# Optimization experiments

Hardware: AMD Instinct MI355X
Metric: run time of the kernel (lower is better)

## Reference

```python
import jax, jax.numpy as jnp
import numpy as np

H = 32  # hidden_size
T = 7   # num_day (seq_len)
F = 1   # num_feature
B = 262144


def _glorot(key, shape):
    # mimic torch uniform(-1/sqrt(H), 1/sqrt(H)) init for LSTM/Linear params
    bound = 1.0 / np.sqrt(H)
    return jax.random.uniform(key, shape, jnp.float32, -bound, bound)


def setup_inputs() -> dict:
    key = jax.random.key(0)
    ks = jax.random.split(key, 14)
    return {
        "inputs": jax.random.normal(ks[0], (B, T, F), jnp.float32),
        # layer 0 (input_size=F)
        "W_ih0": _glorot(ks[1], (4 * H, F)),
        "W_hh0": _glorot(ks[2], (4 * H, H)),
        "b_ih0": _glorot(ks[3], (4 * H,)),
        "b_hh0": _glorot(ks[4], (4 * H,)),
        # layer 1 (input_size=H)
        "W_ih1": _glorot(ks[5], (4 * H, H)),
        "W_hh1": _glorot(ks[6], (4 * H, H)),
        "b_ih1": _glorot(ks[7], (4 * H,)),
        "b_hh1": _glorot(ks[8], (4 * H,)),
        # fc: Linear(H, 1)
        "fc_w": _glorot(ks[9], (1, H)),
        "fc_b": _glorot(ks[10], (1,)),
        # fc1: Linear(T, 1)
        "fc1_w": jax.random.uniform(ks[11], (1, T), jnp.float32, -1.0 / np.sqrt(T), 1.0 / np.sqrt(T)),
        "fc1_b": jax.random.uniform(ks[12], (1,), jnp.float32, -1.0 / np.sqrt(T), 1.0 / np.sqrt(T)),
    }


def _lstm_layer(x_tbf, W_ih, W_hh, b):
    # x_tbf: [T, B, in]; PyTorch gate order: i, f, g, o
    Bdim = x_tbf.shape[1]
    h0 = jnp.zeros((Bdim, H), x_tbf.dtype)
    c0 = jnp.zeros((Bdim, H), x_tbf.dtype)

    def step(carry, x_t):
        h, c = carry
        gates = x_t @ W_ih.T + h @ W_hh.T + b  # [B, 4H]
        i, f, g, o = jnp.split(gates, 4, axis=-1)
        i = jax.nn.sigmoid(i)
        f = jax.nn.sigmoid(f)
        g = jnp.tanh(g)
        o = jax.nn.sigmoid(o)
        c = f * c + i * g
        h = o * jnp.tanh(c)
        return (h, c), h

    _, hs = jax.lax.scan(step, (h0, c0), x_tbf)
    return hs  # [T, B, H]


def reference(inputs, W_ih0, W_hh0, b_ih0, b_hh0, W_ih1, W_hh1, b_ih1, b_hh1,
              fc_w, fc_b, fc1_w, fc1_b):
    x = jnp.transpose(inputs, (1, 0, 2))            # [T, B, F]
    h1 = _lstm_layer(x, W_ih0, W_hh0, b_ih0 + b_hh0)  # [T, B, H]
    h2 = _lstm_layer(h1, W_ih1, W_hh1, b_ih1 + b_hh1)  # [T, B, H]
    out = jnp.transpose(h2, (1, 0, 2))              # [B, T, H]
    y = out @ fc_w.T + fc_b                          # [B, T, 1]
    y = jnp.squeeze(y, 2)                            # [B, T]
    y = y @ fc1_w.T + fc1_b                          # [B, 1]
    return y
```

## Files before the change

### kernel.cpp

```cpp
#include <hip/hip_runtime.h>


#define HID 32
#define TSTEPS 7
#define LSTRIDE 36
#define NWAVES 8

typedef _Float16 half8 __attribute__((ext_vector_type(8)));
typedef float floatx4 __attribute__((ext_vector_type(4)));
typedef float floatx2 __attribute__((ext_vector_type(2)));

#define LOG2E 1.44269504088896f

__device__ __forceinline__ float fast_rcp(float x) { return __builtin_amdgcn_rcpf(x); }

__device__ __forceinline__ float exp2_fast(float x) {
#if __has_builtin(__builtin_amdgcn_exp2f)
    return __builtin_amdgcn_exp2f(x);
#else
    return __expf(x * 0.69314718055994531f);
#endif
}

__device__ __forceinline__ floatx2 mk2(float a, float b) {
    floatx2 v; v[0] = a; v[1] = b; return v;
}
__device__ __forceinline__ floatx2 exp2_v2(floatx2 a) {
    return mk2(exp2_fast(a[0]), exp2_fast(a[1]));
}

__device__ __forceinline__ floatx2 cell_pair(floatx2 gi, floatx2 gf,
                                             floatx2 gg, floatx2 go,
                                             floatx2& cst) {
    const floatx2 one = mk2(1.0f, 1.0f);
    const floatx2 Ea = exp2_v2(gi);
    const floatx2 Db = exp2_v2(gf) + one;
    const floatx2 Ed = exp2_v2(gg);
    const floatx2 Ee = exp2_v2(go);
    const floatx2 M  = (Ea + one) * (Ed + one);
    const float Rb = fast_rcp(Db[0] * Db[1]);
    const float Rm = fast_rcp(M[0] * M[1]);
    const floatx2 ff  = mk2(Rb, Rb) * mk2(Db[1], Db[0]);
    const floatx2 rig = mk2(Rm, Rm) * mk2(M[1], M[0]);
    const floatx2 ig  = __builtin_elementwise_fma(Ed, rig, -rig);
    const floatx2 c   = __builtin_elementwise_fma(ff, cst, ig);
    cst = c;
    const floatx2 Ec  = exp2_v2(c * mk2(2.0f * LOG2E, 2.0f * LOG2E));
    const floatx2 Dh  = (Ee + one) * (Ec + one);
    const float Rh = fast_rcp(Dh[0] * Dh[1]);
    const floatx2 th = mk2(Rh, Rh) * mk2(Dh[1], Dh[0]);
    return __builtin_elementwise_fma(Ec, th, -th);
}

__global__ __launch_bounds__(512, 2) void lstm2_mfma(
    const float* __restrict__ xin,
    const float* __restrict__ Wih0,
    const float* __restrict__ Whh0,
    const float* __restrict__ bih0,
    const float* __restrict__ bhh0,
    const float* __restrict__ Wih1,
    const float* __restrict__ Whh1,
    const float* __restrict__ bih1,
    const float* __restrict__ bhh1,
    const float* __restrict__ fcw,
    const float* __restrict__ fcb,
    const float* __restrict__ fc1w,
    const float* __restrict__ fc1b,
    float* __restrict__ out,
    int B)
{
    const int lane = threadIdx.x & 63;
    const int wave = threadIdx.x >> 6;
    const int col  = lane & 15;
    const int rg   = lane >> 4;
    const int seq_base = (blockIdx.x * NWAVES + wave) * 16;

    __shared__ __align__(16) _Float16 ldsw[3 * 8 * 64 * 8];
    __shared__ __align__(16) floatx2  ldsbw0[128];
    __shared__ float                  ldsb1[128];
    __shared__ __align__(16) _Float16 ldsh[NWAVES][16 * LSTRIDE];
    __shared__ __align__(16) float    ldsx[NWAVES][TSTEPS * 16];

    _Float16* hl = &ldsh[wave][0];
    float* xl = &ldsx[wave][0];

#pragma unroll
    for (int e = lane; e < TSTEPS * 16; e += 64) {
        const int s = e / TSTEPS;
        const int tt = e - s * TSTEPS;
        xl[tt * 16 + s] = xin[seq_base * TSTEPS + e];
    }

    if (wave < 3) {
        const float* Wsrc = (wave == 0) ? Whh0 : (wave == 1) ? Wih1 : Whh1;
#pragma unroll
        for (int nt = 0; nt < 8; ++nt) {
            const int n = nt * 16 + col;
            const float sc = ((n >> 5) == 2) ? (2.0f * LOG2E) : (-LOG2E);
            const float* s = Wsrc + n * HID + rg * 8;
            half8 f;
#pragma unroll
            for (int j = 0; j < 8; ++j) f[j] = (_Float16)(sc * s[j]);
            *(half8*)&ldsw[((wave * 8 + nt) * 64 + lane) * 8] = f;
        }
    } else if (wave == 3) {
#pragma unroll
        for (int i = 0; i < 2; ++i) {
            const int n = i * 64 + lane;
            const float sc = ((n >> 5) == 2) ? (2.0f * LOG2E) : (-LOG2E);
            floatx2 bw;
            bw[0] = sc * (bih0[n] + bhh0[n]);
            bw[1] = sc * Wih0[n];
            ldsbw0[n] = bw;
            ldsb1[n]  = sc * (bih1[n] + bhh1[n]);
        }
    }
    __syncthreads();

    const float fcw_l0 = fcw[col];
    const float fcw_l1 = fcw[16 + col];

    half8 Ah2 = {};
    floatx2 c1v[2][2] = {}, c2v[2][2] = {};
    floatx2 faccv[2] = {};

    floatx4 g0c[8];
    {
        const floatx4 xr0 = *(const floatx4*)&xl[rg * 4];
        const char* bB0p = (const char*)ldsbw0 + col * 8;
#pragma unroll
        for (int nt = 0; nt < 8; ++nt) {
            const floatx2 bw = *(const floatx2*)(bB0p + nt * 128);
#pragma unroll
            for (int r = 0; r < 4; ++r) g0c[nt][r] = fmaf(bw[1], xr0[r], bw[0]);
        }
    }

    for (int t = 0; t < TSTEPS; ++t) {
        unsigned woff = 0;
        asm volatile("" : "+v"(woff));
        const char* wB  = (const char*)ldsw   + lane * 16 + woff;
        const char* bB0 = (const char*)ldsbw0 + col * 8  + woff;
        const char* bB1 = (const char*)ldsb1  + col * 4  + woff;

#pragma unroll
        for (int q = 0; q < 2; ++q) {
#pragma unroll
            for (int rp = 0; rp < 2; ++rp) {
                const floatx2 h = cell_pair(
                    mk2(g0c[0 + q][rp * 2], g0c[0 + q][rp * 2 + 1]),
                    mk2(g0c[2 + q][rp * 2], g0c[2 + q][rp * 2 + 1]),
                    mk2(g0c[4 + q][rp * 2], g0c[4 + q][rp * 2 + 1]),
                    mk2(g0c[6 + q][rp * 2], g0c[6 + q][rp * 2 + 1]),
                    c1v[q][rp]);
                hl[(rg * 4 + rp * 2 + 0) * LSTRIDE + q * 16 + col] = (_Float16)h[0];
                hl[(rg * 4 + rp * 2 + 1) * LSTRIDE + q * 16 + col] = (_Float16)h[1];
            }
        }
        const half8 Ah1 = *(const half8*)&hl[col * LSTRIDE + rg * 8];

        floatx4 g1[8];
#pragma unroll
        for (int nt = 0; nt < 8; ++nt) {
            const float b1  = *(const float*)(bB1 + nt * 64);
            const half8 f1a = *(const half8*)(wB + 8192  + nt * 1024);
            const half8 f1b = *(const half8*)(wB + 16384 + nt * 1024);
            floatx4 c = {b1, b1, b1, b1};
            c = __builtin_amdgcn_mfma_f32_16x16x32_f16(Ah1, f1a, c, 0, 0, 0);
            g1[nt] = __builtin_amdgcn_mfma_f32_16x16x32_f16(Ah2, f1b, c, 0, 0, 0);
        }

        if (t + 1 < TSTEPS) {
            const floatx4 xr = *(const floatx4*)&xl[(t + 1) * 16 + rg * 4];
#pragma unroll
            for (int nt = 0; nt < 8; ++nt) {
                const floatx2 bw = *(const floatx2*)(bB0 + nt * 128);
                const half8 bf   = *(const half8*)(wB + nt * 1024);
                floatx4 c;
#pragma unroll
                for (int r = 0; r < 4; ++r) c[r] = fmaf(bw[1], xr[r], bw[0]);
                g0c[nt] = __builtin_amdgcn_mfma_f32_16x16x32_f16(Ah1, bf, c, 0, 0, 0);
            }
        }

        const float f1t = fc1w[t];
        const float w0 = f1t * fcw_l0;
        const float w1 = f1t * fcw_l1;
#pragma unroll
        for (int q = 0; q < 2; ++q) {
            const float wq = q ? w1 : w0;
            const floatx2 wqv = mk2(wq, wq);
#pragma unroll
            for (int rp = 0; rp < 2; ++rp) {
                const floatx2 h = cell_pair(
                    mk2(g1[0 + q][rp * 2], g1[0 + q][rp * 2 + 1]),
                    mk2(g1[2 + q][rp * 2], g1[2 + q][rp * 2 + 1]),
                    mk2(g1[4 + q][rp * 2], g1[4 + q][rp * 2 + 1]),
                    mk2(g1[6 + q][rp * 2], g1[6 + q][rp * 2 + 1]),
                    c2v[q][rp]);
                faccv[rp] = __builtin_elementwise_fma(wqv, h, faccv[rp]);
                hl[(rg * 4 + rp * 2 + 0) * LSTRIDE + q * 16 + col] = (_Float16)h[0];
                hl[(rg * 4 + rp * 2 + 1) * LSTRIDE + q * 16 + col] = (_Float16)h[1];
            }
        }
        Ah2 = *(const half8*)&hl[col * LSTRIDE + rg * 8];
    }

    float facc[4];
#pragma unroll
    for (int r = 0; r < 4; ++r) facc[r] = faccv[r >> 1][r & 1];
#pragma unroll
    for (int r = 0; r < 4; ++r) {
        float v = facc[r];
        v += __shfl_xor(v, 1);
        v += __shfl_xor(v, 2);
        v += __shfl_xor(v, 4);
        v += __shfl_xor(v, 8);
        facc[r] = v;
    }
    float sum_f1 = 0.f;
#pragma unroll
    for (int t = 0; t < TSTEPS; ++t) sum_f1 += fc1w[t];
    const float tail = fcb[0] * sum_f1 + fc1b[0];

    if (col == 0) {
#pragma unroll
        for (int r = 0; r < 4; ++r)
            out[seq_base + rg * 4 + r] = facc[r] + tail;
    }
}

extern "C" void kernel_launch(void* const* d_in, const int* in_sizes, int n_in,
                              void* d_out, int out_size, void* d_ws, size_t ws_size,
                              hipStream_t stream) {
    const float* xin  = (const float*)d_in[0];
    const float* Wih0 = (const float*)d_in[1];
    const float* Whh0 = (const float*)d_in[2];
    const float* bih0 = (const float*)d_in[3];
    const float* bhh0 = (const float*)d_in[4];
    const float* Wih1 = (const float*)d_in[5];
    const float* Whh1 = (const float*)d_in[6];
    const float* bih1 = (const float*)d_in[7];
    const float* bhh1 = (const float*)d_in[8];
    const float* fcw  = (const float*)d_in[9];
    const float* fcb  = (const float*)d_in[10];
    const float* fc1w = (const float*)d_in[11];
    const float* fc1b = (const float*)d_in[12];
    float* out = (float*)d_out;

    const int B = in_sizes[0] / TSTEPS;
    const int grid = B / (NWAVES * 16);
    lstm2_mfma<<<grid, NWAVES * 64, 0, stream>>>(
        xin, Wih0, Whh0, bih0, bhh0, Wih1, Whh1, bih1, bhh1,
        fcw, fcb, fc1w, fc1b, out, B);
}
```

Baseline: 197.1 us.

## Split LSTM layers across producer/consumer waves with double-buffered hidden state

Each block now processes 64 sequences with 8 waves split into two roles: waves 0-3 compute layer 0 and write h1 into a double-buffered LDS slot, while waves 4-7 consume it to compute layer 1 and the fc reduction. A block-wide barrier each timestep hands h1 from producer to consumer. This pipelines the two layers across waves and lowers per-wave register pressure. In exchange it halves sequences per block, doubles the grid, and adds seven __syncthreads per block.

Result: slower. 203.9 us (+3.4%).

```diff
diff --git a/kernel.cpp b/kernel.cpp
--- a/kernel.cpp
+++ b/kernel.cpp
@@ -4,7 +4,6 @@
 #define HID 32
 #define TSTEPS 7
 #define LSTRIDE 36
-#define NWAVES 8
 
 typedef _Float16 half8 __attribute__((ext_vector_type(8)));
 typedef float floatx4 __attribute__((ext_vector_type(4)));
@@ -71,24 +70,29 @@
 {
     const int lane = threadIdx.x & 63;
     const int wave = threadIdx.x >> 6;
+    const int pair = wave & 3;
+    const int role = wave >> 2;
     const int col  = lane & 15;
     const int rg   = lane >> 4;
-    const int seq_base = (blockIdx.x * NWAVES + wave) * 16;
+    const int seq_base = (blockIdx.x * 4 + pair) * 16;
 
     __shared__ __align__(16) _Float16 ldsw[3 * 8 * 64 * 8];
     __shared__ __align__(16) floatx2  ldsbw0[128];
     __shared__ float                  ldsb1[128];
-    __shared__ __align__(16) _Float16 ldsh[NWAVES][16 * LSTRIDE];
-    __shared__ __align__(16) float    ldsx[NWAVES][TSTEPS * 16];
-
-    _Float16* hl = &ldsh[wave][0];
-    float* xl = &ldsx[wave][0];
-
-#pragma unroll
-    for (int e = lane; e < TSTEPS * 16; e += 64) {
-        const int s = e / TSTEPS;
-        const int tt = e - s * TSTEPS;
-        xl[tt * 16 + s] = xin[seq_base * TSTEPS + e];
+    __shared__ __align__(16) _Float16 ldsh1[4][2][16 * LSTRIDE];
+    __shared__ __align__(16) _Float16 ldsh2[4][16 * LSTRIDE];
+    __shared__ __align__(16) float    ldsx[4][TSTEPS * 16];
+
+    float* xl = &ldsx[pair][0];
+    _Float16* h2l = &ldsh2[pair][0];
+
+    if (role == 0) {
+#pragma unroll
+        for (int e = lane; e < TSTEPS * 16; e += 64) {
+            const int s = e / TSTEPS;
+            const int tt = e - s * TSTEPS;
+            xl[tt * 16 + s] = xin[seq_base * TSTEPS + e];
+        }
     }
 
     if (wave < 3) {
@@ -120,21 +124,9 @@
     const float fcw_l0 = fcw[col];
     const float fcw_l1 = fcw[16 + col];
 
-    half8 Ah2 = {};
-    floatx2 c1v[2][2] = {}, c2v[2][2] = {};
-    floatx2 faccv[2] = {};
-
-    floatx4 g0c[8];
-    {
-        const floatx4 xr0 = *(const floatx4*)&xl[rg * 4];
-        const char* bB0p = (const char*)ldsbw0 + col * 8;
-#pragma unroll
-        for (int nt = 0; nt < 8; ++nt) {
-            const floatx2 bw = *(const floatx2*)(bB0p + nt * 128);
-#pragma unroll
-            for (int r = 0; r < 4; ++r) g0c[nt][r] = fmaf(bw[1], xr0[r], bw[0]);
-        }
-    }
+    half8 Acur = {};
+    floatx2 cv[2][2] = {};
+    floatx2 fv[2] = {};
 
     for (int t = 0; t < TSTEPS; ++t) {
         unsigned woff = 0;
@@ -143,35 +135,10 @@
         const char* bB0 = (const char*)ldsbw0 + col * 8  + woff;
         const char* bB1 = (const char*)ldsb1  + col * 4  + woff;
 
-#pragma unroll
-        for (int q = 0; q < 2; ++q) {
-#pragma unroll
-            for (int rp = 0; rp < 2; ++rp) {
-                const floatx2 h = cell_pair(
-                    mk2(g0c[0 + q][rp * 2], g0c[0 + q][rp * 2 + 1]),
-                    mk2(g0c[2 + q][rp * 2], g0c[2 + q][rp * 2 + 1]),
-                    mk2(g0c[4 + q][rp * 2], g0c[4 + q][rp * 2 + 1]),
-                    mk2(g0c[6 + q][rp * 2], g0c[6 + q][rp * 2 + 1]),
-                    c1v[q][rp]);
-                hl[(rg * 4 + rp * 2 + 0) * LSTRIDE + q * 16 + col] = (_Float16)h[0];
-                hl[(rg * 4 + rp * 2 + 1) * LSTRIDE + q * 16 + col] = (_Float16)h[1];
-            }
-        }
-        const half8 Ah1 = *(const half8*)&hl[col * LSTRIDE + rg * 8];
-
-        floatx4 g1[8];
-#pragma unroll
-        for (int nt = 0; nt < 8; ++nt) {
-            const float b1  = *(const float*)(bB1 + nt * 64);
-            const half8 f1a = *(const half8*)(wB + 8192  + nt * 1024);
-            const half8 f1b = *(const half8*)(wB + 16384 + nt * 1024);
-            floatx4 c = {b1, b1, b1, b1};
-            c = __builtin_amdgcn_mfma_f32_16x16x32_f16(Ah1, f1a, c, 0, 0, 0);
-            g1[nt] = __builtin_amdgcn_mfma_f32_16x16x32_f16(Ah2, f1b, c, 0, 0, 0);
-        }
-
-        if (t + 1 < TSTEPS) {
-            const floatx4 xr = *(const floatx4*)&xl[(t + 1) * 16 + rg * 4];
+        if (role == 0) {
+            _Float16* h1b = &ldsh1[pair][t & 1][0];
+            const floatx4 xr = *(const floatx4*)&xl[t * 16 + rg * 4];
+            floatx4 g[8];
 #pragma unroll
             for (int nt = 0; nt < 8; ++nt) {
                 const floatx2 bw = *(const floatx2*)(bB0 + nt * 128);
@@ -179,54 +146,87 @@
                 floatx4 c;
 #pragma unroll
                 for (int r = 0; r < 4; ++r) c[r] = fmaf(bw[1], xr[r], bw[0]);
-                g0c[nt] = __builtin_amdgcn_mfma_f32_16x16x32_f16(Ah1, bf, c, 0, 0, 0);
-            }
-        }
-
-        const float f1t = fc1w[t];
-        const float w0 = f1t * fcw_l0;
-        const float w1 = f1t * fcw_l1;
-#pragma unroll
-        for (int q = 0; q < 2; ++q) {
-            const float wq = q ? w1 : w0;
-            const floatx2 wqv = mk2(wq, wq);
-#pragma unroll
-            for (int rp = 0; rp < 2; ++rp) {
-                const floatx2 h = cell_pair(
-                    mk2(g1[0 + q][rp * 2], g1[0 + q][rp * 2 + 1]),
-                    mk2(g1[2 + q][rp * 2], g1[2 + q][rp * 2 + 1]),
-                    mk2(g1[4 + q][rp * 2], g1[4 + q][rp * 2 + 1]),
-                    mk2(g1[6 + q][rp * 2], g1[6 + q][rp * 2 + 1]),
-                    c2v[q][rp]);
-                faccv[rp] = __builtin_elementwise_fma(wqv, h, faccv[rp]);
-                hl[(rg * 4 + rp * 2 + 0) * LSTRIDE + q * 16 + col] = (_Float16)h[0];
-                hl[(rg * 4 + rp * 2 + 1) * LSTRIDE + q * 16 + col] = (_Float16)h[1];
-            }
-        }
-        Ah2 = *(const half8*)&hl[col * LSTRIDE + rg * 8];
-    }
-
-    float facc[4];
-#pragma unroll
-    for (int r = 0; r < 4; ++r) facc[r] = faccv[r >> 1][r & 1];
-#pragma unroll
-    for (int r = 0; r < 4; ++r) {
-        float v = facc[r];
-        v += __shfl_xor(v, 1);
-        v += __shfl_xor(v, 2);
-        v += __shfl_xor(v, 4);
-        v += __shfl_xor(v, 8);
-        facc[r] = v;
-    }
-    float sum_f1 = 0.f;
-#pragma unroll
-    for (int t = 0; t < TSTEPS; ++t) sum_f1 += fc1w[t];
-    const float tail = fcb[0] * sum_f1 + fc1b[0];
-
-    if (col == 0) {
-#pragma unroll
-        for (int r = 0; r < 4; ++r)
-            out[seq_base + rg * 4 + r] = facc[r] + tail;
+                g[nt] = __builtin_amdgcn_mfma_f32_16x16x32_f16(Acur, bf, c, 0, 0, 0);
+            }
+#pragma unroll
+            for (int q = 0; q < 2; ++q) {
+#pragma unroll
+                for (int rp = 0; rp < 2; ++rp) {
+                    const floatx2 h = cell_pair(
+                        mk2(g[0 + q][rp * 2], g[0 + q][rp * 2 + 1]),
+                        mk2(g[2 + q][rp * 2], g[2 + q][rp * 2 + 1]),
+                        mk2(g[4 + q][rp * 2], g[4 + q][rp * 2 + 1]),
+                        mk2(g[6 + q][rp * 2], g[6 + q][rp * 2 + 1]),
+                        cv[q][rp]);
+                    h1b[(rg * 4 + rp * 2 + 0) * LSTRIDE + q * 16 + col] = (_Float16)h[0];
+                    h1b[(rg * 4 + rp * 2 + 1) * LSTRIDE + q * 16 + col] = (_Float16)h[1];
+                }
+            }
+            Acur = *(const half8*)&h1b[col * LSTRIDE + rg * 8];
+        }
+
+        __syncthreads();
+
+        if (role == 1) {
+            const _Float16* h1b = &ldsh1[pair][t & 1][0];
+            const half8 Ah1t = *(const half8*)&h1b[col * LSTRIDE + rg * 8];
+            floatx4 g[8];
+#pragma unroll
+            for (int nt = 0; nt < 8; ++nt) {
+                const float b1  = *(const float*)(bB1 + nt * 64);
+                const half8 f1a = *(const half8*)(wB + 8192  + nt * 1024);
+                const half8 f1b = *(const half8*)(wB + 16384 + nt * 1024);
+                floatx4 c = {b1, b1, b1, b1};
+                c = __builtin_amdgcn_mfma_f32_16x16x32_f16(Ah1t, f1a, c, 0, 0, 0);
+                g[nt] = __builtin_amdgcn_mfma_f32_16x16x32_f16(Acur, f1b, c, 0, 0, 0);
+            }
+            const float f1t = fc1w[t];
+            const float w0 = f1t * fcw_l0;
+            const float w1 = f1t * fcw_l1;
+#pragma unroll
+            for (int q = 0; q < 2; ++q) {
+                const float wq = q ? w1 : w0;
+                const floatx2 wqv = mk2(wq, wq);
+#pragma unroll
+                for (int rp = 0; rp < 2; ++rp) {
+                    const floatx2 h = cell_pair(
+                        mk2(g[0 + q][rp * 2], g[0 + q][rp * 2 + 1]),
+                        mk2(g[2 + q][rp * 2], g[2 + q][rp * 2 + 1]),
+                        mk2(g[4 + q][rp * 2], g[4 + q][rp * 2 + 1]),
+                        mk2(g[6 + q][rp * 2], g[6 + q][rp * 2 + 1]),
+                        cv[q][rp]);
+                    fv[rp] = __builtin_elementwise_fma(wqv, h, fv[rp]);
+                    h2l[(rg * 4 + rp * 2 + 0) * LSTRIDE + q * 16 + col] = (_Float16)h[0];
+                    h2l[(rg * 4 + rp * 2 + 1) * LSTRIDE + q * 16 + col] = (_Float16)h[1];
+                }
+            }
+            Acur = *(const half8*)&h2l[col * LSTRIDE + rg * 8];
+        }
+    }
+
+    if (role == 1) {
+        float facc[4];
+#pragma unroll
+        for (int r = 0; r < 4; ++r) facc[r] = fv[r >> 1][r & 1];
+#pragma unroll
+        for (int r = 0; r < 4; ++r) {
+            float v = facc[r];
+            v += __shfl_xor(v, 1);
+            v += __shfl_xor(v, 2);
+            v += __shfl_xor(v, 4);
+            v += __shfl_xor(v, 8);
+            facc[r] = v;
+        }
+        float sum_f1 = 0.f;
+#pragma unroll
+        for (int t = 0; t < TSTEPS; ++t) sum_f1 += fc1w[t];
+        const float tail = fcb[0] * sum_f1 + fc1b[0];
+
+        if (col == 0) {
+#pragma unroll
+            for (int r = 0; r < 4; ++r)
+                out[seq_base + rg * 4 + r] = facc[r] + tail;
+        }
     }
 }
 
@@ -249,8 +249,8 @@
     float* out = (float*)d_out;
 
     const int B = in_sizes[0] / TSTEPS;
-    const int grid = B / (NWAVES * 16);
-    lstm2_mfma<<<grid, NWAVES * 64, 0, stream>>>(
+    const int grid = B / 64;
+    lstm2_mfma<<<grid, 512, 0, stream>>>(
         xin, Wih0, Whh0, bih0, bhh0, Wih1, Whh1, bih1, bhh1,
         fcw, fcb, fc1w, fc1b, out, B);
 }
```
